# Optimization experiments

Measured on AMD Instinct MI355X. Metric: run time of the kernel, lower is better.

The kernel has to match this reference:

```python
import jax, jax.numpy as jnp
import numpy as np

HIDDEN = 5120
N_HEADS = 16           # 128 total heads / DEVICE_NUM=8
Q_LORA = 1536
KV_LORA = 512
NOPE = 128
ROPE = 64
QK_DIM = NOPE + ROPE   # 192
V_DIM = 128
EPS = 1e-6
ROPE_BASE = 10000.0
SCALE_BY_DEVICE = 1.0 / 8.0
SOFTMAX_SCALE = QK_DIM ** -0.5
B, S = 1, 2048


def rms_norm(x, w, eps=EPS):
    v = jnp.mean(jnp.square(x), axis=-1, keepdims=True)
    return x * jax.lax.rsqrt(v + eps) * w


def rotate_half(x):
    h = x.shape[-1] // 2
    return jnp.concatenate([-x[..., h:], x[..., :h]], axis=-1)


def interleave(x):
    # DeepSeek rope layout: view(b,h,s,d//2,2).transpose(-1,-2).reshape(b,h,s,d)
    b, h, s, d = x.shape
    return jnp.swapaxes(x.reshape(b, h, s, d // 2, 2), -1, -2).reshape(b, h, s, d)


def setup_inputs() -> dict:
    key = jax.random.key(0)
    ks = jax.random.split(key, 8)
    w = 0.02
    hidden_states = jax.random.normal(ks[0], (B, S, HIDDEN), dtype=jnp.float32)
    position_ids = jnp.arange(S, dtype=jnp.int64 if jax.config.jax_enable_x64 else jnp.int32)[None, :]
    causal = jnp.tril(jnp.ones((S, S), dtype=bool))
    attention_mask = jnp.where(causal, 0.0, -1e9).astype(jnp.float32)[None, None]
    return {
        'hidden_states': hidden_states,
        'position_ids': position_ids,
        'attention_mask': attention_mask,
        'ln_w': jnp.ones((HIDDEN,), jnp.float32),
        'wq_a': jax.random.normal(ks[1], (Q_LORA, HIDDEN), jnp.float32) * w,
        'q_a_ln_w': jnp.ones((Q_LORA,), jnp.float32),
        'wq_b': jax.random.normal(ks[2], (N_HEADS * QK_DIM, Q_LORA), jnp.float32) * w,
        'wkv_a': jax.random.normal(ks[3], (KV_LORA + ROPE, HIDDEN), jnp.float32) * w,
        'kv_a_ln_w': jnp.ones((KV_LORA,), jnp.float32),
        'wkv_b': jax.random.normal(ks[4], (N_HEADS * (NOPE + V_DIM), KV_LORA), jnp.float32) * w,
        'wo': jax.random.normal(ks[5], (HIDDEN, N_HEADS * V_DIM), jnp.float32) * w,
    }


def reference(hidden_states, position_ids, attention_mask, ln_w, wq_a, q_a_ln_w,
              wq_b, wkv_a, kv_a_ln_w, wkv_b, wo):
    b, s, _ = hidden_states.shape
    residual = hidden_states * SCALE_BY_DEVICE
    h = rms_norm(hidden_states, ln_w)

    # Q low-rank decompression: q_a_proj -> RMSNorm -> q_b_proj
    q = rms_norm(h @ wq_a.T, q_a_ln_w) @ wq_b.T
    q = q.reshape(b, s, N_HEADS, QK_DIM).transpose(0, 2, 1, 3)  # b,h,s,192
    q_nope, q_pe = q[..., :NOPE], q[..., NOPE:]

    # KV low-rank: kv_a_proj_with_mqa -> split -> RMSNorm -> kv_b_proj
    ckv = h @ wkv_a.T                                           # b,s,512+64
    c_kv, k_pe = ckv[..., :KV_LORA], ckv[..., KV_LORA:]
    k_pe = k_pe[:, None, :, :]                                  # b,1,s,64
    kv = rms_norm(c_kv, kv_a_ln_w) @ wkv_b.T
    kv = kv.reshape(b, s, N_HEADS, NOPE + V_DIM).transpose(0, 2, 1, 3)
    k_nope, v = kv[..., :NOPE], kv[..., NOPE:]

    # RoPE (DeepSeek interleaved layout)
    inv_freq = 1.0 / (ROPE_BASE ** (jnp.arange(0, ROPE, 2, dtype=jnp.float32) / ROPE))
    freqs = position_ids.astype(jnp.float32)[..., None] * inv_freq  # b,s,32
    emb = jnp.concatenate([freqs, freqs], axis=-1)                  # b,s,64
    cos = jnp.cos(emb)[:, None]                                     # b,1,s,64
    sin = jnp.sin(emb)[:, None]
    q_pe = interleave(q_pe)
    k_pe = interleave(k_pe)
    q_pe = q_pe * cos + rotate_half(q_pe) * sin
    k_pe = k_pe * cos + rotate_half(k_pe) * sin

    k = jnp.concatenate([k_nope, jnp.broadcast_to(k_pe, (b, N_HEADS, s, ROPE))], axis=-1)
    qf = jnp.concatenate([q_nope, q_pe], axis=-1)

    scores = jnp.einsum('bhqd,bhkd->bhqk', qf, k) * SOFTMAX_SCALE + attention_mask
    attn = jax.nn.softmax(scores.astype(jnp.float32), axis=-1).astype(qf.dtype)
    out = jnp.einsum('bhqk,bhkd->bhqd', attn, v)                    # b,h,s,128
    out = out.transpose(0, 2, 1, 3).reshape(b, s, N_HEADS * V_DIM) @ wo.T

    hidden_states = residual + out
    return (hidden_states.astype(jnp.float32), k.astype(jnp.float32), v.astype(jnp.float32))
```

## Files before the change

### kernel.cpp

```cpp
#include <hip/hip_runtime.h>
#include <hip/hip_bf16.h>

typedef __hip_bfloat16 bf16;
typedef __attribute__((ext_vector_type(8))) short bf16x8;
typedef __attribute__((ext_vector_type(4))) float f32x4;

#define S_LEN   2048
#define HIDDEN  5120
#define NHEADS  16
#define QLORA   1536
#define KVLORA  512
#define QKD     192
#define VD      128
#define QN      (NHEADS*QKD)
#define KVN     (NHEADS*(128+VD))
#define QCKN    2112
#define SM_SCALE 0.07216878364870322f

__device__ __forceinline__ f32x4 mfma16(bf16x8 a, bf16x8 b, f32x4 c) {
  return __builtin_amdgcn_mfma_f32_16x16x32_bf16(a, b, c, 0, 0, 0);
}
__device__ __forceinline__ void g2l16(const void* g, void* l) {
  __builtin_amdgcn_global_load_lds((const __attribute__((address_space(1))) void*)g,
                                   (__attribute__((address_space(3))) void*)l, 16, 0, 0);
}
__device__ __forceinline__ bf16x8 ld8(const bf16* p) { return *(const bf16x8*)p; }

__global__ void zero_f32(float4* __restrict__ p, int n4)
{
  int i = blockIdx.x * 256 + threadIdx.x;
  if (i < n4) p[i] = (float4){0.f, 0.f, 0.f, 0.f};
}

__global__ void cvt_multi(const float* s0, bf16* d0, int n0,
                          const float* s1, bf16* d1, int n1,
                          const float* s2, bf16* d2, int n2,
                          const float* s3, bf16* d3, int n3,
                          const float* s4, bf16* d4, int n4s)
{
  int i = blockIdx.x * 256 + threadIdx.x;
  const float* s; bf16* d;
  if (i < n0) { s = s0; d = d0; }
  else if ((i -= n0) < n1) { s = s1; d = d1; }
  else if ((i -= n1) < n2) { s = s2; d = d2; }
  else if ((i -= n2) < n3) { s = s3; d = d3; }
  else if ((i -= n3) < n4s) { s = s4; d = d4; }
  else return;
  const float4 v = ((const float4*)s)[i];
  union { bf16 b[4]; unsigned long long u; } pk;
  pk.b[0] = __float2bfloat16(v.x);
  pk.b[1] = __float2bfloat16(v.y);
  pk.b[2] = __float2bfloat16(v.z);
  pk.b[3] = __float2bfloat16(v.w);
  *(unsigned long long*)(d + (size_t)i * 4) = pk.u;
}

__global__ void rmsnorm_k(const float* __restrict__ in, int istride, int C,
                          const float* __restrict__ w,
                          bf16* __restrict__ out, int ostride)
{
  const int row = blockIdx.x;
  const float* x = in + (size_t)row * istride;
  float ss = 0.f;
  for (int c = threadIdx.x; c < C; c += 256) { float v = x[c]; ss += v * v; }
  #pragma unroll
  for (int m = 32; m >= 1; m >>= 1) ss += __shfl_xor(ss, m, 64);
  __shared__ float red[4];
  if ((threadIdx.x & 63) == 0) red[threadIdx.x >> 6] = ss;
  __syncthreads();
  ss = red[0] + red[1] + red[2] + red[3];
  const float sc = rsqrtf(ss / (float)C + 1e-6f);
  bf16* o = out + (size_t)row * ostride;
  for (int c = threadIdx.x; c < C; c += 256)
    o[c] = __float2bfloat16(x[c] * sc * w[c]);
}

template<bool RESID, bool CLAMPN, bool ATOMIC>
__global__ __launch_bounds__(256, 2)
void gemm_nt(const bf16* __restrict__ A, const bf16* __restrict__ Bt,
             float* __restrict__ C, int M, int N, int lda, int klen,
             const float* __restrict__ resid, float rscale)
{
  __shared__ bf16 As[128 * 32];
  __shared__ bf16 Bs[128 * 32];
  const int tid = threadIdx.x;
  const int wave = tid >> 6;
  const int lane = tid & 63;
  const int l15 = lane & 15, quad = lane >> 4;
  const int bm = blockIdx.x * 128, bn = blockIdx.y * 128;
  const int kbase = blockIdx.z * klen;
  const int wm = (wave >> 1) * 64, wn = (wave & 1) * 64;

  const int srow = tid >> 2;
  const int scol = (tid & 3) * 8;
  const bf16* Ag0 = A + (size_t)(bm + srow) * lda + kbase + scol;
  const bf16* Ag1 = A + (size_t)(bm + 64 + srow) * lda + kbase + scol;
  int bn0 = bn + srow, bn1 = bn + 64 + srow;
  if (CLAMPN) { bn0 = min(bn0, N - 1); bn1 = min(bn1, N - 1); }
  const bf16* Bg0 = Bt + (size_t)bn0 * lda + kbase + scol;
  const bf16* Bg1 = Bt + (size_t)bn1 * lda + kbase + scol;

  char* AsW = (char*)As + wave * 1024;
  char* BsW = (char*)Bs + wave * 1024;

  f32x4 acc[4][4];
  #pragma unroll
  for (int i = 0; i < 4; i++)
    #pragma unroll
    for (int j = 0; j < 4; j++) acc[i][j] = (f32x4){0.f, 0.f, 0.f, 0.f};

  const int nk = klen >> 5;
  for (int kt = 0; kt < nk; ++kt) {
    const int k0 = kt << 5;
    g2l16(Ag0 + k0, AsW);
    g2l16(Ag1 + k0, AsW + 4096);
    g2l16(Bg0 + k0, BsW);
    g2l16(Bg1 + k0, BsW + 4096);
    __syncthreads();
    bf16x8 af[4], bfr[4];
    #pragma unroll
    for (int i = 0; i < 4; i++) af[i] = ld8(As + (wm + i * 16 + l15) * 32 + quad * 8);
    #pragma unroll
    for (int j = 0; j < 4; j++) bfr[j] = ld8(Bs + (wn + j * 16 + l15) * 32 + quad * 8);
    #pragma unroll
    for (int i = 0; i < 4; i++)
      #pragma unroll
      for (int j = 0; j < 4; j++)
        acc[i][j] = mfma16(af[i], bfr[j], acc[i][j]);
    __syncthreads();
  }

  #pragma unroll
  for (int i = 0; i < 4; i++)
    #pragma unroll
    for (int j = 0; j < 4; j++) {
      const int row = bm + wm + i * 16 + quad * 4;
      const int col = bn + wn + j * 16 + l15;
      if (!CLAMPN || col < N) {
        #pragma unroll
        for (int r = 0; r < 4; r++) {
          float v = acc[i][j][r];
          const size_t idx = (size_t)(row + r) * N + col;
          if (RESID) v += resid[idx] * rscale;
          if (ATOMIC) unsafeAtomicAdd(&C[idx], v);
          else        C[idx] = v;
        }
      }
    }
}

__global__ void rope_assemble_k(
    const float* __restrict__ q,
    const float* __restrict__ qackv,
    const float* __restrict__ kv,
    const int*   __restrict__ pos,
    float* __restrict__ k_out,
    bf16*  __restrict__ q_bf,
    bf16*  __restrict__ k_bf)
{
  const int s = blockIdx.x;
  const int t = threadIdx.x;
  __shared__ float cs[32], sn[32], kpe[64];
  const float p = (float)pos[s];
  if (t < 32) {
    const float inv = powf(10000.0f, -((float)(2 * t)) / 64.0f);
    const float f = p * inv;
    float si, c;
    sincosf(f, &si, &c);
    cs[t] = c; sn[t] = si;
    const float r0v = qackv[(size_t)s * QCKN + 2048 + 2 * t];
    const float r1v = qackv[(size_t)s * QCKN + 2048 + 2 * t + 1];
    kpe[t]      = r0v * c - r1v * si;
    kpe[32 + t] = r1v * c + r0v * si;
  }
  __syncthreads();
  for (int i = t; i < NHEADS * 128; i += 256) {
    const int h = i >> 7, d = i & 127;
    const size_t o = ((size_t)h * S_LEN + s) * QKD + d;
    const float kn = kv[(size_t)s * KVN + h * 256 + d];
    k_out[o] = kn;
    k_bf[o] = __float2bfloat16(kn);
    q_bf[o] = __float2bfloat16(q[(size_t)s * QN + h * QKD + d]);
  }
  for (int i = t; i < NHEADS * 32; i += 256) {
    const int h = i >> 5, jj = i & 31;
    const float r0v = q[(size_t)s * QN + h * QKD + 128 + 2 * jj];
    const float r1v = q[(size_t)s * QN + h * QKD + 128 + 2 * jj + 1];
    const float c = cs[jj], si = sn[jj];
    const size_t o = ((size_t)h * S_LEN + s) * QKD + 128;
    q_bf[o + jj]      = __float2bfloat16(r0v * c - r1v * si);
    q_bf[o + 32 + jj] = __float2bfloat16(r1v * c + r0v * si);
  }
  for (int i = t; i < NHEADS * 64; i += 256) {
    const int h = i >> 6, jj = i & 63;
    const float v = kpe[jj];
    const size_t o = ((size_t)h * S_LEN + s) * QKD + 128 + jj;
    k_out[o] = v;
    k_bf[o] = __float2bfloat16(v);
  }
}

__global__ void v_transpose_k(const float* __restrict__ kv,
                              float* __restrict__ v_out,
                              bf16* __restrict__ vt_bf)
{
  const int h = blockIdx.x, st = blockIdx.y, dt = blockIdx.z;
  __shared__ float tile[32][33];
  const int tx = threadIdx.x & 31;
  const int ty = (threadIdx.x >> 5) * 4;
  const int s0 = st * 32, d0 = dt * 32;
  #pragma unroll
  for (int r = 0; r < 4; r++) {
    const int sl = ty + r;
    const float v = kv[(size_t)(s0 + sl) * KVN + h * 256 + 128 + d0 + tx];
    v_out[((size_t)h * S_LEN + s0 + sl) * VD + d0 + tx] = v;
    tile[sl][tx] = v;
  }
  __syncthreads();
  #pragma unroll
  for (int r = 0; r < 4; r++) {
    const int dl = ty + r;
    vt_bf[((size_t)h * VD + d0 + dl) * S_LEN + s0 + tx] = __float2bfloat16(tile[tx][dl]);
  }
}

__global__ __launch_bounds__(256, 3)
void attn_k(const bf16* __restrict__ qb, const bf16* __restrict__ kb,
            const bf16* __restrict__ vt, bf16* __restrict__ aout)
{
  const int head = blockIdx.y;
  const int qt = (head < 8) ? blockIdx.x : (gridDim.x - 1 - blockIdx.x);
  const int wave = threadIdx.x >> 6, lane = threadIdx.x & 63;
  const int l15 = lane & 15, quad = lane >> 4;
  const int r0 = qt * 64 + wave * 16;

  const bf16* qh = qb + (size_t)head * S_LEN * QKD;
  const bf16* kh = kb + (size_t)head * S_LEN * QKD;
  const bf16* vh = vt + (size_t)head * VD * S_LEN;

  __shared__ bf16 Ks[6 * 64 * 32];
  __shared__ bf16 Vs[128 * 72];
  __shared__ bf16 Plds[4][16][72];

  const int tid = threadIdx.x;
  const int srow = wave * 16 + (lane >> 2);
  const int scol = (lane & 3) * 8;
  const bf16* ksrc = kh + (size_t)srow * QKD + scol;
  bf16* kdst = Ks + srow * 32 + scol;
  const int vrow = tid >> 1;
  const int vcol = (tid & 1) * 32;
  const bf16* vsrc = vh + (size_t)vrow * S_LEN + vcol;
  bf16* vdst = Vs + vrow * 72 + vcol;

  bf16x8 qf[6];
  #pragma unroll
  for (int c = 0; c < 6; ++c)
    qf[c] = ld8(qh + (size_t)(r0 + l15) * QKD + c * 32 + quad * 8);

  f32x4 O[8];
  #pragma unroll
  for (int d = 0; d < 8; ++d) O[d] = (f32x4){0.f, 0.f, 0.f, 0.f};
  float mrow[4] = {-1e30f, -1e30f, -1e30f, -1e30f};
  float lrow[4] = {0.f, 0.f, 0.f, 0.f};

  bf16x8 kreg[6], vreg[4];
  #pragma unroll
  for (int c = 0; c < 6; ++c) kreg[c] = ld8(ksrc + c * 32);
  #pragma unroll
  for (int c = 0; c < 4; ++c) vreg[c] = ld8(vsrc + c * 8);

  for (int j = 0; j <= qt; ++j) {
    __syncthreads();
    #pragma unroll
    for (int c = 0; c < 6; ++c) *(bf16x8*)(kdst + c * 2048) = kreg[c];
    #pragma unroll
    for (int c = 0; c < 4; ++c) *(bf16x8*)(vdst + c * 8) = vreg[c];
    __syncthreads();
    if (j < qt) {
      const bf16* src = ksrc + (size_t)(j + 1) * 64 * QKD;
      #pragma unroll
      for (int c = 0; c < 6; ++c) kreg[c] = ld8(src + c * 32);
      const bf16* vs2 = vsrc + (size_t)(j + 1) * 64;
      #pragma unroll
      for (int c = 0; c < 4; ++c) vreg[c] = ld8(vs2 + c * 8);
    }
    const int kc = j * 64;

    f32x4 S[4];
    #pragma unroll
    for (int nt = 0; nt < 4; ++nt) S[nt] = (f32x4){0.f, 0.f, 0.f, 0.f};
    #pragma unroll
    for (int c = 0; c < 6; ++c) {
      #pragma unroll
      for (int nt = 0; nt < 4; ++nt) {
        const bf16x8 kf = ld8(Ks + c * 2048 + (nt * 16 + l15) * 32 + quad * 8);
        S[nt] = mfma16(qf[c], kf, S[nt]);
      }
    }

    float mnew[4] = {-1e30f, -1e30f, -1e30f, -1e30f};
    if (j == qt) {
      #pragma unroll
      for (int nt = 0; nt < 4; ++nt) {
        const int col = kc + nt * 16 + l15;
        #pragma unroll
        for (int r = 0; r < 4; r++) {
          const int row = r0 + quad * 4 + r;
          const float v = (col <= row) ? S[nt][r] * SM_SCALE : -1e30f;
          S[nt][r] = v;
          mnew[r] = fmaxf(mnew[r], v);
        }
      }
    } else {
      #pragma unroll
      for (int nt = 0; nt < 4; ++nt)
        #pragma unroll
        for (int r = 0; r < 4; r++) {
          const float v = S[nt][r] * SM_SCALE;
          S[nt][r] = v;
          mnew[r] = fmaxf(mnew[r], v);
        }
    }
    #pragma unroll
    for (int m = 8; m >= 1; m >>= 1)
      #pragma unroll
      for (int r = 0; r < 4; r++)
        mnew[r] = fmaxf(mnew[r], __shfl_xor(mnew[r], m, 64));
    float alpha[4], ladd[4] = {0.f, 0.f, 0.f, 0.f};
    #pragma unroll
    for (int r = 0; r < 4; r++) {
      const float mi = fmaxf(mrow[r], mnew[r]);
      alpha[r] = __expf(mrow[r] - mi);
      mrow[r] = mi;
    }
    #pragma unroll
    for (int nt = 0; nt < 4; ++nt)
      #pragma unroll
      for (int r = 0; r < 4; r++) {
        const float pv = __expf(S[nt][r] - mrow[r]);
        S[nt][r] = pv;
        ladd[r] += pv;
      }
    #pragma unroll
    for (int m = 8; m >= 1; m >>= 1)
      #pragma unroll
      for (int r = 0; r < 4; r++) ladd[r] += __shfl_xor(ladd[r], m, 64);
    #pragma unroll
    for (int r = 0; r < 4; r++) lrow[r] = lrow[r] * alpha[r] + ladd[r];
    #pragma unroll
    for (int d = 0; d < 8; ++d)
      #pragma unroll
      for (int r = 0; r < 4; r++) O[d][r] *= alpha[r];

    #pragma unroll
    for (int nt = 0; nt < 4; ++nt)
      #pragma unroll
      for (int r = 0; r < 4; r++)
        Plds[wave][quad * 4 + r][nt * 16 + l15] = __float2bfloat16(S[nt][r]);

    #pragma unroll
    for (int kt = 0; kt < 2; ++kt) {
      const bf16x8 pf = ld8(&Plds[wave][l15][kt * 32 + quad * 8]);
      #pragma unroll
      for (int dt = 0; dt < 8; ++dt) {
        const bf16x8 vf = ld8(Vs + (dt * 16 + l15) * 72 + kt * 32 + quad * 8);
        O[dt] = mfma16(pf, vf, O[dt]);
      }
    }
  }

  #pragma unroll
  for (int dt = 0; dt < 8; ++dt) {
    const int col = head * VD + dt * 16 + l15;
    #pragma unroll
    for (int r = 0; r < 4; r++) {
      const int row = r0 + quad * 4 + r;
      aout[(size_t)row * (NHEADS * VD) + col] = __float2bfloat16(O[dt][r] / lrow[r]);
    }
  }
}

extern "C" void kernel_launch(void* const* d_in, const int* in_sizes, int n_in,
                              void* d_out, int out_size, void* d_ws, size_t ws_size,
                              hipStream_t stream)
{
  const float* hs      = (const float*)d_in[0];
  const int*   pos     = (const int*)  d_in[1];
  const float* ln_w    = (const float*)d_in[3];
  const float* wq_a    = (const float*)d_in[4];
  const float* q_a_ln  = (const float*)d_in[5];
  const float* wq_b    = (const float*)d_in[6];
  const float* wkv_a   = (const float*)d_in[7];
  const float* kv_a_ln = (const float*)d_in[8];
  const float* wkv_b   = (const float*)d_in[9];
  const float* wo      = (const float*)d_in[10];

  float* out_hidden = (float*)d_out;
  float* out_k = out_hidden + (size_t)S_LEN * HIDDEN;
  float* out_v = out_k + (size_t)NHEADS * S_LEN * QKD;

  char* ws = (char*)d_ws;
  size_t off = 0;
  auto alloc = [&](size_t bytes) { char* p = ws + off; off += (bytes + 255) & ~255ULL; return p; };

  bf16* h_b     = (bf16*)alloc((size_t)S_LEN * HIDDEN * 2);
  bf16* w1_b    = (bf16*)alloc((size_t)QCKN * HIDDEN * 2);
  bf16* wqb_b   = (bf16*)alloc((size_t)QN * QLORA * 2);
  bf16* wkvb_b  = (bf16*)alloc((size_t)KVN * KVLORA * 2);
  bf16* wo_b    = (bf16*)alloc((size_t)HIDDEN * (NHEADS * VD) * 2);
  float* qa_ckv = (float*)alloc((size_t)S_LEN * QCKN * 4);
  float* q_f    = (float*)alloc((size_t)S_LEN * QN * 4);
  bf16* qa_n    = (bf16*)alloc((size_t)S_LEN * QLORA * 2);
  bf16* ckv_n   = (bf16*)alloc((size_t)S_LEN * KVLORA * 2);
  float* kv_f   = (float*)alloc((size_t)S_LEN * KVN * 4);
  bf16* q_bf    = (bf16*)alloc((size_t)NHEADS * S_LEN * QKD * 2);
  bf16* k_bf    = (bf16*)alloc((size_t)NHEADS * S_LEN * QKD * 2);
  bf16* vt_bf   = (bf16*)alloc((size_t)NHEADS * VD * S_LEN * 2);
  bf16* attn_b  = (bf16*)alloc((size_t)S_LEN * (NHEADS * VD) * 2);

  {
    const int n4 = (int)(((size_t)S_LEN * QCKN + (size_t)S_LEN * QN) / 4);
    zero_f32<<<(n4 + 255) / 256, 256, 0, stream>>>((float4*)qa_ckv, n4);
  }

  {
    const int n0 = (QLORA * HIDDEN) / 4;
    const int n1 = ((QCKN - QLORA) * HIDDEN) / 4;
    const int n2 = (QN * QLORA) / 4;
    const int n3 = (KVN * KVLORA) / 4;
    const int n4s = (HIDDEN * NHEADS * VD) / 4;
    const int tot = n0 + n1 + n2 + n3 + n4s;
    cvt_multi<<<(tot + 255) / 256, 256, 0, stream>>>(
        wq_a, w1_b, n0,
        wkv_a, w1_b + (size_t)QLORA * HIDDEN, n1,
        wq_b, wqb_b, n2,
        wkv_b, wkvb_b, n3,
        wo, wo_b, n4s);
  }

  rmsnorm_k<<<S_LEN, 256, 0, stream>>>(hs, HIDDEN, HIDDEN, ln_w, h_b, HIDDEN);

  gemm_nt<false, true, true><<<dim3(16, 17, 4), 256, 0, stream>>>(
      h_b, w1_b, qa_ckv, S_LEN, QCKN, HIDDEN, HIDDEN / 4, nullptr, 0.f);

  rmsnorm_k<<<S_LEN, 256, 0, stream>>>(qa_ckv, QCKN, QLORA, q_a_ln, qa_n, QLORA);
  rmsnorm_k<<<S_LEN, 256, 0, stream>>>(qa_ckv + QLORA, QCKN, KVLORA, kv_a_ln, ckv_n, KVLORA);

  gemm_nt<false, false, true><<<dim3(16, QN / 128, 2), 256, 0, stream>>>(
      qa_n, wqb_b, q_f, S_LEN, QN, QLORA, QLORA / 2, nullptr, 0.f);
  gemm_nt<false, false, false><<<dim3(16, KVN / 128, 1), 256, 0, stream>>>(
      ckv_n, wkvb_b, kv_f, S_LEN, KVN, KVLORA, KVLORA, nullptr, 0.f);

  rope_assemble_k<<<S_LEN, 256, 0, stream>>>(q_f, qa_ckv, kv_f, pos, out_k, q_bf, k_bf);
  v_transpose_k<<<dim3(NHEADS, S_LEN / 32, VD / 32), 256, 0, stream>>>(kv_f, out_v, vt_bf);

  attn_k<<<dim3(S_LEN / 64, NHEADS), 256, 0, stream>>>(q_bf, k_bf, vt_bf, attn_b);

  gemm_nt<true, false, false><<<dim3(16, HIDDEN / 128, 1), 256, 0, stream>>>(
      attn_b, wo_b, out_hidden, S_LEN, HIDDEN, NHEADS * VD, NHEADS * VD, hs, 0.125f);

  (void)in_sizes; (void)n_in; (void)out_size; (void)ws_size;
}
```

Before: 605.5 us.

## Double GEMM k-tile to 64 and split-K the output projection with atomics

The GEMM now stages two 32-wide k chunks per iteration, which halves the number of barrier pairs per k and gives more MFMA work between syncs, at the cost of doubling LDS per block. The output projection switches from a fused residual epilogue to split-K by 2 with atomic adds. Its output buffer is pre-initialised to hidden_states*0.125 inside a merged init kernel that also zeroes the other accumulators. This adds parallelism for the wo GEMM but adds atomic traffic and an extra full-size read and write of the output.

```diff
diff --git a/kernel.cpp b/kernel.cpp
--- a/kernel.cpp
+++ b/kernel.cpp
@@ -26,10 +26,18 @@
 }
 __device__ __forceinline__ bf16x8 ld8(const bf16* p) { return *(const bf16x8*)p; }
 
-__global__ void zero_f32(float4* __restrict__ p, int n4)
+__global__ void init_k(float4* __restrict__ qa_ckv, int n_qa,
+                       float4* __restrict__ q_f, int n_q,
+                       const float4* __restrict__ hs, float4* __restrict__ oh, int n_h)
 {
   int i = blockIdx.x * 256 + threadIdx.x;
-  if (i < n4) p[i] = (float4){0.f, 0.f, 0.f, 0.f};
+  if (i < n_qa) { qa_ckv[i] = (float4){0.f, 0.f, 0.f, 0.f}; return; }
+  if ((i -= n_qa) < n_q) { q_f[i] = (float4){0.f, 0.f, 0.f, 0.f}; return; }
+  if ((i -= n_q) < n_h) {
+    float4 v = hs[i];
+    v.x *= 0.125f; v.y *= 0.125f; v.z *= 0.125f; v.w *= 0.125f;
+    oh[i] = v;
+  }
 }
 
 __global__ void cvt_multi(const float* s0, bf16* d0, int n0,
@@ -75,14 +83,13 @@
     o[c] = __float2bfloat16(x[c] * sc * w[c]);
 }
 
-template<bool RESID, bool CLAMPN, bool ATOMIC>
+template<bool CLAMPN, bool ATOMIC>
 __global__ __launch_bounds__(256, 2)
 void gemm_nt(const bf16* __restrict__ A, const bf16* __restrict__ Bt,
-             float* __restrict__ C, int M, int N, int lda, int klen,
-             const float* __restrict__ resid, float rscale)
-{
-  __shared__ bf16 As[128 * 32];
-  __shared__ bf16 Bs[128 * 32];
+             float* __restrict__ C, int M, int N, int lda, int klen)
+{
+  __shared__ bf16 As[2 * 128 * 32];
+  __shared__ bf16 Bs[2 * 128 * 32];
   const int tid = threadIdx.x;
   const int wave = tid >> 6;
   const int lane = tid & 63;
@@ -109,24 +116,32 @@
     #pragma unroll
     for (int j = 0; j < 4; j++) acc[i][j] = (f32x4){0.f, 0.f, 0.f, 0.f};
 
-  const int nk = klen >> 5;
+  const int nk = klen >> 6;
   for (int kt = 0; kt < nk; ++kt) {
-    const int k0 = kt << 5;
-    g2l16(Ag0 + k0, AsW);
-    g2l16(Ag1 + k0, AsW + 4096);
-    g2l16(Bg0 + k0, BsW);
-    g2l16(Bg1 + k0, BsW + 4096);
+    const int k0 = kt << 6;
+    #pragma unroll
+    for (int c = 0; c < 2; ++c) {
+      g2l16(Ag0 + k0 + c * 32, AsW + c * 8192);
+      g2l16(Ag1 + k0 + c * 32, AsW + c * 8192 + 4096);
+      g2l16(Bg0 + k0 + c * 32, BsW + c * 8192);
+      g2l16(Bg1 + k0 + c * 32, BsW + c * 8192 + 4096);
+    }
     __syncthreads();
-    bf16x8 af[4], bfr[4];
-    #pragma unroll
-    for (int i = 0; i < 4; i++) af[i] = ld8(As + (wm + i * 16 + l15) * 32 + quad * 8);
-    #pragma unroll
-    for (int j = 0; j < 4; j++) bfr[j] = ld8(Bs + (wn + j * 16 + l15) * 32 + quad * 8);
-    #pragma unroll
-    for (int i = 0; i < 4; i++)
+    #pragma unroll
+    for (int c = 0; c < 2; ++c) {
+      bf16x8 af[4], bfr[4];
+      #pragma unroll
+      for (int i = 0; i < 4; i++)
+        af[i] = ld8(As + c * 4096 + (wm + i * 16 + l15) * 32 + quad * 8);
       #pragma unroll
       for (int j = 0; j < 4; j++)
-        acc[i][j] = mfma16(af[i], bfr[j], acc[i][j]);
+        bfr[j] = ld8(Bs + c * 4096 + (wn + j * 16 + l15) * 32 + quad * 8);
+      #pragma unroll
+      for (int i = 0; i < 4; i++)
+        #pragma unroll
+        for (int j = 0; j < 4; j++)
+          acc[i][j] = mfma16(af[i], bfr[j], acc[i][j]);
+    }
     __syncthreads();
   }
 
@@ -139,9 +154,8 @@
       if (!CLAMPN || col < N) {
         #pragma unroll
         for (int r = 0; r < 4; r++) {
-          float v = acc[i][j][r];
+          const float v = acc[i][j][r];
           const size_t idx = (size_t)(row + r) * N + col;
-          if (RESID) v += resid[idx] * rscale;
           if (ATOMIC) unsafeAtomicAdd(&C[idx], v);
           else        C[idx] = v;
         }
@@ -419,8 +433,13 @@
   bf16* attn_b  = (bf16*)alloc((size_t)S_LEN * (NHEADS * VD) * 2);
 
   {
-    const int n4 = (int)(((size_t)S_LEN * QCKN + (size_t)S_LEN * QN) / 4);
-    zero_f32<<<(n4 + 255) / 256, 256, 0, stream>>>((float4*)qa_ckv, n4);
+    const int n_qa = (int)((size_t)S_LEN * QCKN / 4);
+    const int n_q  = (int)((size_t)S_LEN * QN / 4);
+    const int n_h  = (int)((size_t)S_LEN * HIDDEN / 4);
+    const int tot = n_qa + n_q + n_h;
+    init_k<<<(tot + 255) / 256, 256, 0, stream>>>(
+        (float4*)qa_ckv, n_qa, (float4*)q_f, n_q,
+        (const float4*)hs, (float4*)out_hidden, n_h);
   }
 
   {
@@ -440,24 +459,24 @@
 
   rmsnorm_k<<<S_LEN, 256, 0, stream>>>(hs, HIDDEN, HIDDEN, ln_w, h_b, HIDDEN);
 
-  gemm_nt<false, true, true><<<dim3(16, 17, 4), 256, 0, stream>>>(
-      h_b, w1_b, qa_ckv, S_LEN, QCKN, HIDDEN, HIDDEN / 4, nullptr, 0.f);
+  gemm_nt<true, true><<<dim3(16, 17, 4), 256, 0, stream>>>(
+      h_b, w1_b, qa_ckv, S_LEN, QCKN, HIDDEN, HIDDEN / 4);
 
   rmsnorm_k<<<S_LEN, 256, 0, stream>>>(qa_ckv, QCKN, QLORA, q_a_ln, qa_n, QLORA);
   rmsnorm_k<<<S_LEN, 256, 0, stream>>>(qa_ckv + QLORA, QCKN, KVLORA, kv_a_ln, ckv_n, KVLORA);
 
-  gemm_nt<false, false, true><<<dim3(16, QN / 128, 2), 256, 0, stream>>>(
-      qa_n, wqb_b, q_f, S_LEN, QN, QLORA, QLORA / 2, nullptr, 0.f);
-  gemm_nt<false, false, false><<<dim3(16, KVN / 128, 1), 256, 0, stream>>>(
-      ckv_n, wkvb_b, kv_f, S_LEN, KVN, KVLORA, KVLORA, nullptr, 0.f);
+  gemm_nt<false, true><<<dim3(16, QN / 128, 2), 256, 0, stream>>>(
+      qa_n, wqb_b, q_f, S_LEN, QN, QLORA, QLORA / 2);
+  gemm_nt<false, false><<<dim3(16, KVN / 128, 1), 256, 0, stream>>>(
+      ckv_n, wkvb_b, kv_f, S_LEN, KVN, KVLORA, KVLORA);
 
   rope_assemble_k<<<S_LEN, 256, 0, stream>>>(q_f, qa_ckv, kv_f, pos, out_k, q_bf, k_bf);
   v_transpose_k<<<dim3(NHEADS, S_LEN / 32, VD / 32), 256, 0, stream>>>(kv_f, out_v, vt_bf);
 
   attn_k<<<dim3(S_LEN / 64, NHEADS), 256, 0, stream>>>(q_bf, k_bf, vt_bf, attn_b);
 
-  gemm_nt<true, false, false><<<dim3(16, HIDDEN / 128, 1), 256, 0, stream>>>(
-      attn_b, wo_b, out_hidden, S_LEN, HIDDEN, NHEADS * VD, NHEADS * VD, hs, 0.125f);
+  gemm_nt<false, true><<<dim3(16, HIDDEN / 128, 2), 256, 0, stream>>>(
+      attn_b, wo_b, out_hidden, S_LEN, HIDDEN, NHEADS * VD, (NHEADS * VD) / 2);
 
   (void)in_sizes; (void)n_in; (void)out_size; (void)ws_size;
 }
```

New measurement: 627.6 us. 1.04x slower.
